# Performance work log

Hardware: AMD Instinct MI355X
Metric: run time of the kernel (lower is better)

The kernel has to match this reference:

```python
import jax, jax.numpy as jnp
import numpy as np

N, E = 50000, 800000
F_IN, C_PRE, C, G_HID = 16, 32, 64, 64
EPS = 1e-5


def graph_norm(x, batch, w, b, ms):
    # PyG GraphNorm over a single graph (batch all zeros)
    cnt = jax.ops.segment_sum(jnp.ones((x.shape[0], 1), x.dtype), batch, num_segments=1)
    mean = jax.ops.segment_sum(x, batch, num_segments=1) / cnt
    out = x - mean[batch] * ms
    var = jax.ops.segment_sum(out * out, batch, num_segments=1) / cnt
    std = jnp.sqrt(var + EPS)
    return w * out / std[batch] + b


def ggnn_conv(h, edge_index, edge_attr,
              gw1, gb1, gw2, gb2, gw3, gb3,
              zw, zb, rw, rb, hw, hb):
    n = h.shape[0]
    loops = jnp.arange(n)
    row = jnp.concatenate([edge_index[0], loops])  # sources (x_j)
    col = jnp.concatenate([edge_index[1], loops])  # targets (x_i), aggregation index
    ea = jnp.concatenate([edge_attr, jnp.ones((n, 1), h.dtype)], axis=0)
    deg = jax.ops.segment_sum(jnp.ones(col.shape[0], h.dtype), col, num_segments=n)
    dis = jnp.where(deg > 0, deg ** -0.5, 0.0)
    norm = dis[row] * dis[col]
    x_j = h[row]
    x_i = h[col]
    g = jnp.concatenate([x_i, x_j, ea], axis=-1)            # [E+N, 2C+1]
    g = jax.nn.relu(g @ gw1 + gb1)
    g = jax.nn.relu(g @ gw2 + gb2)
    gate = jax.nn.sigmoid(g @ gw3 + gb3)                     # [E+N, 1]
    msg = gate * (norm[:, None] * x_j)
    aggr = jax.ops.segment_sum(msg, col, num_segments=n)     # scatter-add
    zi = jnp.concatenate([h, aggr], axis=-1)
    z = jax.nn.sigmoid(zi @ zw + zb)
    r = jax.nn.sigmoid(zi @ rw + rb)
    hc = jax.nn.relu(jnp.concatenate([r * h, aggr], axis=-1) @ hw + hb)
    return (1.0 - z) * h + z * hc


def setup_inputs() -> dict:
    key = jax.random.key(0)
    ks = iter(jax.random.split(key, 40))

    def lin(k, fi, fo):
        return jax.random.normal(k, (fi, fo), jnp.float32) / np.sqrt(fi)

    inp = {
        'x': jax.random.normal(next(ks), (N, F_IN), jnp.float32),
        'edge_index': jax.random.randint(next(ks), (2, E), 0, N),
        'edge_attr': jax.random.uniform(next(ks), (E, 1), jnp.float32),
        'batch': jnp.zeros((N,), jnp.int32),
        'preproc_w': lin(next(ks), F_IN, C_PRE), 'preproc_b': jnp.zeros((C_PRE,), jnp.float32),
        'gn_pre_w': jnp.ones((C_PRE,), jnp.float32), 'gn_pre_b': jnp.zeros((C_PRE,), jnp.float32), 'gn_pre_ms': jnp.ones((C_PRE,), jnp.float32),
        'init_w': lin(next(ks), C_PRE, C), 'init_b': jnp.zeros((C,), jnp.float32),
        'gn_init_w': jnp.ones((C,), jnp.float32), 'gn_init_b': jnp.zeros((C,), jnp.float32), 'gn_init_ms': jnp.ones((C,), jnp.float32),
        'gate_w1': lin(next(ks), 2 * C + 1, G_HID), 'gate_b1': jnp.zeros((G_HID,), jnp.float32),
        'gate_w2': lin(next(ks), G_HID, G_HID), 'gate_b2': jnp.zeros((G_HID,), jnp.float32),
        'gate_w3': lin(next(ks), G_HID, 1), 'gate_b3': jnp.zeros((1,), jnp.float32),
        'lin_z_w': lin(next(ks), 2 * C, C), 'lin_z_b': jnp.zeros((C,), jnp.float32),
        'lin_r_w': lin(next(ks), 2 * C, C), 'lin_r_b': jnp.zeros((C,), jnp.float32),
        'lin_h_w': lin(next(ks), 2 * C, C), 'lin_h_b': jnp.zeros((C,), jnp.float32),
        'gn_ggnn_w': jnp.ones((C,), jnp.float32), 'gn_ggnn_b': jnp.zeros((C,), jnp.float32), 'gn_ggnn_ms': jnp.ones((C,), jnp.float32),
        'fc1_w': lin(next(ks), 2 * C, C), 'fc1_b': jnp.zeros((C,), jnp.float32),
        'gn_fc1_w': jnp.ones((C,), jnp.float32), 'gn_fc1_b': jnp.zeros((C,), jnp.float32), 'gn_fc1_ms': jnp.ones((C,), jnp.float32),
        'fc2_w': lin(next(ks), C, 2), 'fc2_b': jnp.zeros((2,), jnp.float32),
    }
    return inp


def reference(x, edge_index, edge_attr, batch,
              preproc_w, preproc_b, gn_pre_w, gn_pre_b, gn_pre_ms,
              init_w, init_b, gn_init_w, gn_init_b, gn_init_ms,
              gate_w1, gate_b1, gate_w2, gate_b2, gate_w3, gate_b3,
              lin_z_w, lin_z_b, lin_r_w, lin_r_b, lin_h_w, lin_h_b,
              gn_ggnn_w, gn_ggnn_b, gn_ggnn_ms,
              fc1_w, fc1_b, gn_fc1_w, gn_fc1_b, gn_fc1_ms,
              fc2_w, fc2_b):
    n_layers = 4
    h = x @ preproc_w + preproc_b
    h = graph_norm(h, batch, gn_pre_w, gn_pre_b, gn_pre_ms)
    h = jax.nn.relu(h)
    h0 = h @ init_w + init_b
    h0 = graph_norm(h0, batch, gn_init_w, gn_init_b, gn_init_ms)
    h0 = jax.nn.relu(h0)
    h = h0
    for _ in range(n_layers):  # tied GGNN layer
        h = ggnn_conv(h, edge_index, edge_attr,
                      gate_w1, gate_b1, gate_w2, gate_b2, gate_w3, gate_b3,
                      lin_z_w, lin_z_b, lin_r_w, lin_r_b, lin_h_w, lin_h_b)
        h = graph_norm(h, batch, gn_ggnn_w, gn_ggnn_b, gn_ggnn_ms)
    out = jnp.concatenate([h0, h], axis=1)
    out = out @ fc1_w + fc1_b
    out = graph_norm(out, batch, gn_fc1_w, gn_fc1_b, gn_fc1_ms)
    out = jax.nn.relu(out)
    out = out @ fc2_w + fc2_b  # [N, 2] logits
    return out
```

## Files before the change

kernel.cpp:

```cpp
#include <hip/hip_runtime.h>

#define GN_EPS 1e-5f

typedef _Float16 half8 __attribute__((ext_vector_type(8)));
typedef float floatx4 __attribute__((ext_vector_type(4)));

__device__ __forceinline__ float sigmoidf_(float x){ return 1.0f/(1.0f+__expf(-x)); }
__device__ __forceinline__ float bcast_(float v, int k){
  return __int_as_float(__builtin_amdgcn_readlane(__float_as_int(v), k));
}

__global__ void cnt_all_kernel(const int* __restrict__ ei, int* cnt, int E, int n){
  int i = blockIdx.x*blockDim.x+threadIdx.x;
  if (i < n) atomicAdd(&cnt[i], 1);
  if (i < E) atomicAdd(&cnt[ei[E+i]], 1);
}
__global__ __launch_bounds__(256) void scan1_kernel(const int* __restrict__ cnt,
                                                    int* loc, int* bsum,
                                                    float* __restrict__ dis, int n){
  __shared__ int s[256];
  int t = threadIdx.x, i = blockIdx.x*256 + t;
  int v = (i < n) ? cnt[i] : 0;
  if (i < n) dis[i] = rsqrtf((float)v);
  s[t] = v; __syncthreads();
  #pragma unroll
  for (int d = 1; d < 256; d <<= 1){
    int u = (t >= d) ? s[t-d] : 0; __syncthreads();
    s[t] += u; __syncthreads();
  }
  if (i < n) loc[i] = s[t] - v;
  if (t == 255) bsum[blockIdx.x] = s[255];
}
__global__ __launch_bounds__(256) void scan2_kernel(int* bsum, int nb){
  __shared__ int s[256];
  int t = threadIdx.x;
  int v = (t < nb) ? bsum[t] : 0;
  s[t] = v; __syncthreads();
  #pragma unroll
  for (int d = 1; d < 256; d <<= 1){
    int u = (t >= d) ? s[t-d] : 0; __syncthreads();
    s[t] += u; __syncthreads();
  }
  if (t < nb) bsum[t] = s[t] - v;
}
__global__ void scan3_kernel(const int* __restrict__ loc, const int* __restrict__ bsum,
                             int* rowptr, int* fill, int n, int total){
  int i = blockIdx.x*blockDim.x+threadIdx.x;
  if (i < n){ rowptr[i] = loc[i] + bsum[i >> 8]; fill[i] = 0; }
  if (i == 0) rowptr[n] = total;
}
__global__ void scatter_kernel(const int* __restrict__ ei, const float* __restrict__ ea,
                               const int* __restrict__ rowptr, int* fill,
                               unsigned* sd, _Float16* ea2, int E, int n){
  int idx = blockIdx.x*blockDim.x+threadIdx.x;
  int tot = E + n;
  if (idx >= tot) return;
  int r, c; float v;
  if (idx < E){ r = ei[idx]; c = ei[E+idx]; v = ea[idx]; }
  else        { r = c = idx - E; v = 1.0f; }
  int j = rowptr[c] + atomicAdd(&fill[c], 1);
  sd[j] = (unsigned)r | ((unsigned)c << 16);
  ea2[j] = (_Float16)v;
}

__global__ __launch_bounds__(256) void wprep_kernel(
    const float* __restrict__ w1, const float* __restrict__ zw,
    const float* __restrict__ rw, const float* __restrict__ hw,
    const float* __restrict__ fw, const float* __restrict__ w2,
    _Float16* __restrict__ wp){
  int idx = blockIdx.x*256 + threadIdx.x;
  if (idx < 8192){
    int t=idx>>10, kh=(idx>>9)&1, g=(idx>>7)&3, l=(idx>>3)&15, j=idx&7;
    int kg=(t>=4?64:0)+kh*32+g*8+j;
    wp[idx] = (_Float16)w1[kg*64 + (t&3)*16 + l];
  } else if (idx < 40960){
    int m=(idx-8192)>>13, k=(idx-8192)&8191;
    int t=(k>>11)&3, kh=(k>>9)&3, g=(k>>7)&3, l=(k>>3)&15, j=k&7;
    const float* W = (m==0)?zw:((m==1)?rw:((m==2)?hw:fw));
    wp[idx] = (_Float16)W[(kh*32+g*8+j)*64 + t*16 + l];
  } else if (idx < 45056){
    int k = idx-40960;
    int t=(k>>10)&3, kh=(k>>9)&1, g=(k>>7)&3, l=(k>>3)&15, j=k&7;
    wp[idx] = (_Float16)w2[(kh*32+g*8+j)*64 + t*16 + l];
  }
}

template<int K_IN, int C_OUT, int STATS>
__global__ __launch_bounds__(256) void mm1_kernel(
    const float* __restrict__ x, const float* __restrict__ W,
    const float* __restrict__ b, float* __restrict__ y,
    float* __restrict__ stats, int n){
  __shared__ float sW[K_IN*C_OUT];
  __shared__ float sSt[2*C_OUT];
  if (STATS && threadIdx.x < 2*C_OUT) sSt[threadIdx.x] = 0.f;
  for (int i = threadIdx.x; i < K_IN*C_OUT; i += 256) sW[i] = W[i];
  __syncthreads();
  const int lane = threadIdx.x & 63;
  const int col  = (lane < C_OUT) ? lane : 0;
  const float bias = b[col];
  int wid = (blockIdx.x*256 + threadIdx.x) >> 6;
  int nw  = (gridDim.x*256) >> 6;
  float qs = 0.f, qq = 0.f;
  for (int i = wid; i < n; i += nw){
    float xv = (lane < K_IN) ? x[(size_t)i*K_IN + lane] : 0.0f;
    float a0 = bias, a1 = 0.0f;
    #pragma unroll
    for (int k = 0; k < K_IN; k += 2){
      a0 += bcast_(xv, k  ) * sW[(k  )*C_OUT + col];
      a1 += bcast_(xv, k+1) * sW[(k+1)*C_OUT + col];
    }
    if (lane < C_OUT){
      float v = a0 + a1;
      y[(size_t)i*C_OUT + lane] = v;
      if (STATS){ qs += v; qq += v*v; }
    }
  }
  if (STATS){
    if (lane < C_OUT){
      atomicAdd(&sSt[lane], qs);
      atomicAdd(&sSt[C_OUT+lane], qq);
    }
    __syncthreads();
    if (threadIdx.x < 2*C_OUT) atomicAdd(&stats[threadIdx.x], sSt[threadIdx.x]);
  }
}

template<int RELU, int WRITE_H0>
__global__ __launch_bounds__(256) void normpq_kernel(
    const float* __restrict__ hin, float* __restrict__ hout,
    float* __restrict__ h0out,
    const float* __restrict__ stats,
    const float* __restrict__ gw, const float* __restrict__ gb,
    const float* __restrict__ gms,
    const _Float16* __restrict__ w1p, const float* __restrict__ b1,
    _Float16* __restrict__ Ph, _Float16* __restrict__ QH, int n)
{
  __shared__ _Float16 sB[8192];
  __shared__ float sSO[128];
  for (int i = threadIdx.x; i < 1024; i += 256)
    ((half8*)sB)[i] = ((const half8*)w1p)[i];
  if (threadIdx.x < 64){
    int ch = threadIdx.x;
    float invN = 1.0f/(float)n;
    float mean = stats[ch]*invN;
    float mm = mean*gms[ch];
    float var = stats[64+ch]*invN - mm*(2.0f*mean - mm);
    float inv = rsqrtf(fmaxf(var,0.f)+GN_EPS);
    float sc = inv*gw[ch];
    sSO[ch] = sc;
    sSO[64+ch] = gb[ch] - mm*sc;
  }
  __syncthreads();
  const int lane = threadIdx.x & 63;
  const int g16 = lane>>4, l16 = lane&15;
  float scA[8], ofA[8], scB[8], ofB[8];
  #pragma unroll
  for (int j = 0; j < 8; ++j){
    scA[j]=sSO[g16*8+j];    ofA[j]=sSO[64+g16*8+j];
    scB[j]=sSO[32+g16*8+j]; ofB[j]=sSO[96+g16*8+j];
  }
  float b1f[4];
  #pragma unroll
  for (int t = 0; t < 4; ++t) b1f[t] = b1[t*16 + l16];

  int wid = (blockIdx.x*blockDim.x + threadIdx.x) >> 6;
  int nw  = (gridDim.x*blockDim.x) >> 6;
  int tiles = (n + 15) >> 4;
  for (int tile = wid; tile < tiles; tile += nw){
    int base = tile*16;
    int na = min(base + l16, n-1);
    const float* hp = hin + (size_t)na*64;
    float4 a0 = *(const float4*)(hp + g16*8);
    float4 a1 = *(const float4*)(hp + g16*8 + 4);
    float4 c0 = *(const float4*)(hp + 32 + g16*8);
    float4 c1 = *(const float4*)(hp + 32 + g16*8 + 4);
    float va[8] = {a0.x,a0.y,a0.z,a0.w,a1.x,a1.y,a1.z,a1.w};
    float vb[8] = {c0.x,c0.y,c0.z,c0.w,c1.x,c1.y,c1.z,c1.w};
    half8 af0, af1;
    #pragma unroll
    for (int j = 0; j < 8; ++j){
      float v = va[j]*scA[j] + ofA[j];
      if (RELU) v = fmaxf(v, 0.f);
      va[j] = v; af0[j] = (_Float16)v;
      float u = vb[j]*scB[j] + ofB[j];
      if (RELU) u = fmaxf(u, 0.f);
      vb[j] = u; af1[j] = (_Float16)u;
    }
    float* op = hout + (size_t)na*64;
    *(float4*)(op + g16*8)       = (float4){va[0],va[1],va[2],va[3]};
    *(float4*)(op + g16*8 + 4)   = (float4){va[4],va[5],va[6],va[7]};
    *(float4*)(op + 32 + g16*8)  = (float4){vb[0],vb[1],vb[2],vb[3]};
    *(float4*)(op + 32 + g16*8+4)= (float4){vb[4],vb[5],vb[6],vb[7]};
    if (WRITE_H0){
      float* o2 = h0out + (size_t)na*64;
      *(float4*)(o2 + g16*8)       = (float4){va[0],va[1],va[2],va[3]};
      *(float4*)(o2 + g16*8 + 4)   = (float4){va[4],va[5],va[6],va[7]};
      *(float4*)(o2 + 32 + g16*8)  = (float4){vb[0],vb[1],vb[2],vb[3]};
      *(float4*)(o2 + 32 + g16*8+4)= (float4){vb[4],vb[5],vb[6],vb[7]};
    }
    *(half8*)(QH + (size_t)na*128 + 64 + g16*8) = af0;
    *(half8*)(QH + (size_t)na*128 + 96 + g16*8) = af1;

    floatx4 acc[8];
    #pragma unroll
    for (int t = 0; t < 8; ++t){
      float bv = (t < 4) ? b1f[t] : 0.0f;
      acc[t] = (floatx4){bv, bv, bv, bv};
    }
    #pragma unroll
    for (int t = 0; t < 8; ++t){
      half8 bf0 = *(const half8*)&sB[((t*2+0)*4+g16)*128 + l16*8];
      half8 bf1 = *(const half8*)&sB[((t*2+1)*4+g16)*128 + l16*8];
      acc[t] = __builtin_amdgcn_mfma_f32_16x16x32_f16(af0, bf0, acc[t], 0, 0, 0);
      acc[t] = __builtin_amdgcn_mfma_f32_16x16x32_f16(af1, bf1, acc[t], 0, 0, 0);
    }
    #pragma unroll
    for (int t = 0; t < 8; ++t)
      #pragma unroll
      for (int rg = 0; rg < 4; ++rg){
        int nd = base + g16*4 + rg;
        if (nd < n){
          if (t < 4) Ph[(size_t)nd*64  + t*16 + l16]      = (_Float16)acc[t][rg];
          else       QH[(size_t)nd*128 + (t-4)*16 + l16]  = (_Float16)acc[t][rg];
        }
      }
  }
}

__global__ __launch_bounds__(256) void gru_mfma_kernel(
    float* __restrict__ h, float* __restrict__ aggr,
    const float* __restrict__ dis, const _Float16* __restrict__ QH,
    const _Float16* __restrict__ gwp,
    const float* __restrict__ zb, const float* __restrict__ rb,
    const float* __restrict__ hb,
    float* __restrict__ stats, int n)
{
  __shared__ _Float16 sW[3*8192];
  __shared__ _Float16 sRH[4][16][72];
  __shared__ float sSt[128];
  if (threadIdx.x < 128) sSt[threadIdx.x] = 0.f;
  for (int i = threadIdx.x; i < 3072; i += 256)
    ((half8*)sW)[i] = ((const half8*)gwp)[i];
  __syncthreads();
  const int lane = threadIdx.x & 63;
  const int g16 = lane>>4, l16 = lane&15;
  const int w = threadIdx.x >> 6;
  float zbf[4], rbf[4], hbf[4];
  #pragma unroll
  for (int t = 0; t < 4; ++t){
    zbf[t] = zb[t*16+l16]; rbf[t] = rb[t*16+l16]; hbf[t] = hb[t*16+l16];
  }
  float ssum[4] = {0,0,0,0}, ssq[4] = {0,0,0,0};
#define GW(m,t,kh) (*(const half8*)&sW[(m)*8192 + (((t)*4+(kh))*4+g16)*128 + l16*8])

  int wid = (blockIdx.x*blockDim.x + threadIdx.x) >> 6;
  int nw  = (gridDim.x*blockDim.x) >> 6;
  int tiles = (n + 15) >> 4;
  for (int tile = wid; tile < tiles; tile += nw){
    int base = tile*16;
    int na = min(base + l16, n-1);
    float dv = dis[na];
    half8 af[4];
    af[0] = *(const half8*)(QH + (size_t)na*128 + 64 + g16*8);
    af[1] = *(const half8*)(QH + (size_t)na*128 + 96 + g16*8);
    #pragma unroll
    for (int kh = 0; kh < 2; ++kh){
      float* ar = aggr + (size_t)na*64 + kh*32 + g16*8;
      float4 a0 = *(const float4*)ar;
      float4 a1 = *(const float4*)(ar+4);
      *(float4*)(ar)   = (float4){0,0,0,0};
      *(float4*)(ar+4) = (float4){0,0,0,0};
      half8 t8;
      t8[0]=(_Float16)(a0.x*dv); t8[1]=(_Float16)(a0.y*dv);
      t8[2]=(_Float16)(a0.z*dv); t8[3]=(_Float16)(a0.w*dv);
      t8[4]=(_Float16)(a1.x*dv); t8[5]=(_Float16)(a1.y*dv);
      t8[6]=(_Float16)(a1.z*dv); t8[7]=(_Float16)(a1.w*dv);
      af[2+kh] = t8;
    }
    floatx4 az[4], ar4[4];
    #pragma unroll
    for (int t = 0; t < 4; ++t){
      az[t]  = (floatx4){zbf[t], zbf[t], zbf[t], zbf[t]};
      ar4[t] = (floatx4){rbf[t], rbf[t], rbf[t], rbf[t]};
      #pragma unroll
      for (int kh = 0; kh < 4; ++kh){
        az[t]  = __builtin_amdgcn_mfma_f32_16x16x32_f16(af[kh], GW(0,t,kh), az[t],  0, 0, 0);
        ar4[t] = __builtin_amdgcn_mfma_f32_16x16x32_f16(af[kh], GW(1,t,kh), ar4[t], 0, 0, 0);
      }
    }
    float zr[16], hv[16];
    #pragma unroll
    for (int t = 0; t < 4; ++t)
      #pragma unroll
      for (int rg = 0; rg < 4; ++rg){
        int ndc = min(base + g16*4 + rg, n-1);
        float hval = h[(size_t)ndc*64 + t*16 + l16];
        float zv = sigmoidf_(az[t][rg]);
        float rv = sigmoidf_(ar4[t][rg]);
        zr[t*4+rg] = zv; hv[t*4+rg] = hval;
        sRH[w][g16*4+rg][t*16+l16] = (_Float16)(rv*hval);
      }
    asm volatile("s_waitcnt lgkmcnt(0)" ::: "memory");
    __builtin_amdgcn_sched_barrier(0);
    half8 af2_0 = *(const half8*)&sRH[w][l16][g16*8];
    half8 af2_1 = *(const half8*)&sRH[w][l16][32 + g16*8];
    floatx4 ah[4];
    #pragma unroll
    for (int t = 0; t < 4; ++t){
      ah[t] = (floatx4){hbf[t], hbf[t], hbf[t], hbf[t]};
      ah[t] = __builtin_amdgcn_mfma_f32_16x16x32_f16(af2_0, GW(2,t,0), ah[t], 0, 0, 0);
      ah[t] = __builtin_amdgcn_mfma_f32_16x16x32_f16(af2_1, GW(2,t,1), ah[t], 0, 0, 0);
      ah[t] = __builtin_amdgcn_mfma_f32_16x16x32_f16(af[2],  GW(2,t,2), ah[t], 0, 0, 0);
      ah[t] = __builtin_amdgcn_mfma_f32_16x16x32_f16(af[3],  GW(2,t,3), ah[t], 0, 0, 0);
    }
    #pragma unroll
    for (int t = 0; t < 4; ++t)
      #pragma unroll
      for (int rg = 0; rg < 4; ++rg){
        int nd = base + g16*4 + rg;
        if (nd < n){
          float hc = fmaxf(ah[t][rg], 0.f);
          float zv = zr[t*4+rg];
          float hn = (1.f - zv)*hv[t*4+rg] + zv*hc;
          h[(size_t)nd*64 + t*16 + l16] = hn;
          ssum[t] += hn; ssq[t] += hn*hn;
        }
      }
  }
#undef GW
  #pragma unroll
  for (int t = 0; t < 4; ++t){
    atomicAdd(&sSt[t*16+l16], ssum[t]);
    atomicAdd(&sSt[64+t*16+l16], ssq[t]);
  }
  __syncthreads();
  if (threadIdx.x < 128) atomicAdd(&stats[threadIdx.x], sSt[threadIdx.x]);
}

__global__ __launch_bounds__(256) void fc1_mfma_kernel(
    const float* __restrict__ h0, const float* __restrict__ h,
    const _Float16* __restrict__ fp, const float* __restrict__ b,
    float* __restrict__ out, float* __restrict__ stats, int n)
{
  __shared__ _Float16 sB[8192];
  __shared__ float sSt[128];
  if (threadIdx.x < 128) sSt[threadIdx.x] = 0.f;
  for (int i = threadIdx.x; i < 1024; i += 256)
    ((half8*)sB)[i] = ((const half8*)fp)[i];
  __syncthreads();
  const int lane = threadIdx.x & 63;
  const int g16 = lane>>4, l16 = lane&15;
  float bf[4];
  #pragma unroll
  for (int t = 0; t < 4; ++t) bf[t] = b[t*16+l16];
  float ssum[4] = {0,0,0,0}, ssq[4] = {0,0,0,0};

  int wid = (blockIdx.x*blockDim.x + threadIdx.x) >> 6;
  int nw  = (gridDim.x*blockDim.x) >> 6;
  int tiles = (n + 15) >> 4;
  for (int tile = wid; tile < tiles; tile += nw){
    int base = tile*16;
    int na = min(base + l16, n-1);
    half8 af[4];
    #pragma unroll
    for (int kh = 0; kh < 4; ++kh){
      const float* sp = (kh < 2 ? h0 : h) + (size_t)na*64 + (kh&1)*32 + g16*8;
      float4 a0 = *(const float4*)sp;
      float4 a1 = *(const float4*)(sp+4);
      half8 t8;
      t8[0]=(_Float16)a0.x; t8[1]=(_Float16)a0.y; t8[2]=(_Float16)a0.z; t8[3]=(_Float16)a0.w;
      t8[4]=(_Float16)a1.x; t8[5]=(_Float16)a1.y; t8[6]=(_Float16)a1.z; t8[7]=(_Float16)a1.w;
      af[kh] = t8;
    }
    #pragma unroll
    for (int t = 0; t < 4; ++t){
      floatx4 acc = (floatx4){bf[t], bf[t], bf[t], bf[t]};
      #pragma unroll
      for (int kh = 0; kh < 4; ++kh)
        acc = __builtin_amdgcn_mfma_f32_16x16x32_f16(af[kh],
                *(const half8*)&sB[((t*4+kh)*4+g16)*128 + l16*8], acc, 0, 0, 0);
      #pragma unroll
      for (int rg = 0; rg < 4; ++rg){
        int nd = base + g16*4 + rg;
        if (nd < n){
          float v = acc[rg];
          out[(size_t)nd*64 + t*16 + l16] = v;
          ssum[t] += v; ssq[t] += v*v;
        }
      }
    }
  }
  #pragma unroll
  for (int t = 0; t < 4; ++t){
    atomicAdd(&sSt[t*16+l16], ssum[t]);
    atomicAdd(&sSt[64+t*16+l16], ssq[t]);
  }
  __syncthreads();
  if (threadIdx.x < 128) atomicAdd(&stats[threadIdx.x], sSt[threadIdx.x]);
}

__global__ __launch_bounds__(256) void edge_tile_kernel(
    const unsigned* __restrict__ sd, const _Float16* __restrict__ ea2,
    const _Float16* __restrict__ Ph, const _Float16* __restrict__ QH,
    const float* __restrict__ dis,
    const _Float16* __restrict__ w2p, const float* __restrict__ b2,
    const float* __restrict__ w1e, const float* __restrict__ w3,
    const float* __restrict__ b3,
    float* __restrict__ aggr, float* __restrict__ stats, int EN)
{
  __shared__ _Float16 sB[4096];
  if (blockIdx.x == 0 && threadIdx.x < 128) stats[threadIdx.x] = 0.f;
  for (int i = threadIdx.x; i < 512; i += 256)
    ((half8*)sB)[i] = ((const half8*)w2p)[i];
  __syncthreads();

  const int lane = threadIdx.x & 63;
  const int g16  = lane >> 4;
  const int l16  = lane & 15;

  half8 w1h[2];
  #pragma unroll
  for (int kh = 0; kh < 2; ++kh)
    #pragma unroll
    for (int j = 0; j < 8; ++j)
      w1h[kh][j] = (_Float16)w1e[kh*32 + g16*8 + j];

  float w3f[4], b2f[4];
  #pragma unroll
  for (int t = 0; t < 4; ++t){ w3f[t] = w3[t*16 + l16]; b2f[t] = b2[t*16 + l16]; }
  const float b3v = b3[0];
  const _Float16* QHh = QH + 64;

  int wid = (blockIdx.x*blockDim.x + threadIdx.x) >> 6;
  int nw  = (gridDim.x*blockDim.x) >> 6;
  int tiles = (EN + 15) >> 4;

  for (int tile = wid; tile < tiles; tile += nw){
    int e0 = tile << 4;
    int m = EN - e0; if (m > 16) m = 16;
    int el = e0 + ((l16 < m) ? l16 : (m-1));
    unsigned sdv = sd[el];
    int r = (int)(sdv & 0xffffu);
    int c = (int)(sdv >> 16);
    float dv = (l16 < m) ? dis[r] : 0.0f;
    _Float16 eavh = ea2[el];

    half8 hq0 = *(const half8*)(QH + (size_t)r*128 + g16*8);
    half8 hq1 = *(const half8*)(QH + (size_t)r*128 + 32 + g16*8);
    half8 p0  = *(const half8*)(Ph + (size_t)c*64 + g16*8);
    half8 p1  = *(const half8*)(Ph + (size_t)c*64 + 32 + g16*8);

    _Float16 hv16[16];
    #pragma unroll
    for (int i = 0; i < 16; ++i){
      int ri = __builtin_amdgcn_readlane(r, i);
      hv16[i] = QHh[(size_t)ri*128 + lane];
    }

    half8 e8;
    #pragma unroll
    for (int j = 0; j < 8; ++j) e8[j] = eavh;
    half8 a0h = p0 + hq0 + w1h[0]*e8;
    half8 a1h = p1 + hq1 + w1h[1]*e8;
    #pragma unroll
    for (int j = 0; j < 8; ++j){
      a0h[j] = a0h[j] > (_Float16)0.f ? a0h[j] : (_Float16)0.f;
      a1h[j] = a1h[j] > (_Float16)0.f ? a1h[j] : (_Float16)0.f;
    }

    floatx4 acc[4];
    #pragma unroll
    for (int t4 = 0; t4 < 4; ++t4)
      acc[t4] = (floatx4){b2f[t4], b2f[t4], b2f[t4], b2f[t4]};
    __builtin_amdgcn_s_setprio(1);
    #pragma unroll
    for (int t4 = 0; t4 < 4; ++t4){
      half8 bf0 = *(const half8*)&sB[t4*1024 + g16*128 + l16*8];
      half8 bf1 = *(const half8*)&sB[t4*1024 + 512 + g16*128 + l16*8];
      acc[t4] = __builtin_amdgcn_mfma_f32_16x16x32_f16(a0h, bf0, acc[t4], 0, 0, 0);
      acc[t4] = __builtin_amdgcn_mfma_f32_16x16x32_f16(a1h, bf1, acc[t4], 0, 0, 0);
    }
    __builtin_amdgcn_s_setprio(0);

    float s[4] = {0.f,0.f,0.f,0.f};
    #pragma unroll
    for (int t4 = 0; t4 < 4; ++t4)
      #pragma unroll
      for (int rg = 0; rg < 4; ++rg)
        s[rg] += fmaxf(acc[t4][rg], 0.0f) * w3f[t4];
    #pragma unroll
    for (int rg = 0; rg < 4; ++rg){
      #pragma unroll
      for (int off = 1; off < 16; off <<= 1)
        s[rg] += __shfl_xor(s[rg], off);
      s[rg] = sigmoidf_(s[rg] + b3v);
    }

    float fs[4];
    #pragma unroll
    for (int rg = 0; rg < 4; ++rg){
      float dvp = __shfl(dv, (g16 << 4) | (g16*4 + rg));
      fs[rg] = s[rg] * dvp;
    }

    int cnext = __shfl(c, (lane & 48) | ((l16 + 1) & 15));
    unsigned long long bm = __ballot(c != cnext);
    unsigned bmask = ((unsigned)bm | 0x8000u) & 0xffffu;

    float accv = 0.f;
    #pragma unroll
    for (int i = 0; i < 16; ++i){
      float gi = bcast_(fs[i & 3], (i >> 2) << 4);
      accv = fmaf(gi, (float)hv16[i], accv);
      if ((bmask >> i) & 1){
        int ci = __builtin_amdgcn_readlane(c, i);
        atomicAdd(&aggr[(size_t)ci*64 + lane], accv);
        accv = 0.f;
      }
    }
  }
}

template<int C, int RELU>
__global__ __launch_bounds__(256) void norm_apply_kernel(
    const float* __restrict__ x, const float* __restrict__ stats,
    const float* __restrict__ w, const float* __restrict__ b,
    const float* __restrict__ ms, float* __restrict__ y, int n){
  const float invN = 1.0f / (float)n;
  size_t idx = blockIdx.x*256 + threadIdx.x;
  size_t step = (size_t)gridDim.x*256;
  size_t tot = (size_t)n*C;
  for (; idx < tot; idx += step){
    int c = idx % C;
    float mean = stats[c] * invN;
    float mm = mean * ms[c];
    float var = stats[C + c]*invN - mm*(2.0f*mean - mm);
    float inv = rsqrtf(fmaxf(var, 0.0f) + GN_EPS);
    float v = (x[idx] - mm)*inv*w[c] + b[c];
    if (RELU) v = fmaxf(v, 0.0f);
    y[idx] = v;
  }
}

__global__ void fc2_kernel(
    const float* __restrict__ x, const float* __restrict__ w,
    const float* __restrict__ b, float* __restrict__ out, int n){
  int i = blockIdx.x*blockDim.x + threadIdx.x;
  if (i >= n) return;
  float a0 = b[0], a1 = b[1];
  const float4* xr = (const float4*)(x + (size_t)i*64);
  #pragma unroll
  for (int k4 = 0; k4 < 16; ++k4){
    float4 v = xr[k4];
    int k = k4*4;
    a0 += v.x*w[(k+0)*2+0] + v.y*w[(k+1)*2+0] + v.z*w[(k+2)*2+0] + v.w*w[(k+3)*2+0];
    a1 += v.x*w[(k+0)*2+1] + v.y*w[(k+1)*2+1] + v.z*w[(k+2)*2+1] + v.w*w[(k+3)*2+1];
  }
  out[i*2+0] = a0;
  out[i*2+1] = a1;
}

extern "C" void kernel_launch(void* const* d_in, const int* in_sizes, int n_in,
                              void* d_out, int out_size, void* d_ws, size_t ws_size,
                              hipStream_t stream){
  const float* x          = (const float*)d_in[0];
  const int*   ei         = (const int*)  d_in[1];
  const float* ea         = (const float*)d_in[2];
  const float* preproc_w  = (const float*)d_in[4];
  const float* preproc_b  = (const float*)d_in[5];
  const float* gn_pre_w   = (const float*)d_in[6];
  const float* gn_pre_b   = (const float*)d_in[7];
  const float* gn_pre_ms  = (const float*)d_in[8];
  const float* init_w     = (const float*)d_in[9];
  const float* init_b     = (const float*)d_in[10];
  const float* gn_init_w  = (const float*)d_in[11];
  const float* gn_init_b  = (const float*)d_in[12];
  const float* gn_init_ms = (const float*)d_in[13];
  const float* gate_w1    = (const float*)d_in[14];
  const float* gate_b1    = (const float*)d_in[15];
  const float* gate_w2    = (const float*)d_in[16];
  const float* gate_b2    = (const float*)d_in[17];
  const float* gate_w3    = (const float*)d_in[18];
  const float* gate_b3    = (const float*)d_in[19];
  const float* lin_z_w    = (const float*)d_in[20];
  const float* lin_z_b    = (const float*)d_in[21];
  const float* lin_r_w    = (const float*)d_in[22];
  const float* lin_r_b    = (const float*)d_in[23];
  const float* lin_h_w    = (const float*)d_in[24];
  const float* lin_h_b    = (const float*)d_in[25];
  const float* gn_ggnn_w  = (const float*)d_in[26];
  const float* gn_ggnn_b  = (const float*)d_in[27];
  const float* gn_ggnn_ms = (const float*)d_in[28];
  const float* fc1_w      = (const float*)d_in[29];
  const float* fc1_b      = (const float*)d_in[30];
  const float* gn_fc1_w   = (const float*)d_in[31];
  const float* gn_fc1_b   = (const float*)d_in[32];
  const float* gn_fc1_ms  = (const float*)d_in[33];
  const float* fc2_w      = (const float*)d_in[34];
  const float* fc2_b      = (const float*)d_in[35];

  const int N = in_sizes[3];
  const int E = in_sizes[1] / 2;
  const int EN = E + N;

  float* base = (float*)d_ws;
  const size_t R = (size_t)64*N;
  float* h     = base;
  float* h0    = h    + R;
  float* Preg  = h0   + R;
  float* aggr  = Preg + R;
  float* QHreg = aggr + R;
  float* dis   = QHreg + R;
  float* stats = dis + N;
  size_t need = (5*R + N + 128) * sizeof(float);
  if (ws_size < need || N > 65535) return;

  _Float16* Ph  = (_Float16*)Preg;
  _Float16* QH  = (_Float16*)QHreg;
  unsigned* sd  = (unsigned*)(Preg + 32*(size_t)N);
  _Float16* ea2 = (_Float16*)(sd + EN);
  _Float16* wp  = (_Float16*)(((uintptr_t)(ea2 + EN) + 15) & ~(uintptr_t)15);
  _Float16* w1p = wp;
  _Float16* gwp = wp + 8192;
  _Float16* fc1p= wp + 32768;
  _Float16* w2p = wp + 40960;

  int* cnt    = (int*)aggr;
  int* loc    = cnt + N;
  int* fill   = loc + N;
  int* bsum   = fill + N;
  int* rowptr = bsum + 256;

  const int GB = 1024;
  const int RB = 784;
  const int EB = 3072;
  const int nb = (N + 255) / 256;
  const int mNE = (E > N ? E : N);

  hipMemsetAsync(cnt, 0, (size_t)N*sizeof(int), stream);
  cnt_all_kernel<<<(mNE+255)/256, 256, 0, stream>>>(ei, cnt, E, N);
  scan1_kernel<<<nb, 256, 0, stream>>>(cnt, loc, bsum, dis, N);
  scan2_kernel<<<1, 256, 0, stream>>>(bsum, nb);
  scan3_kernel<<<nb, 256, 0, stream>>>(loc, bsum, rowptr, fill, N, EN);
  scatter_kernel<<<(EN+255)/256, 256, 0, stream>>>(ei, ea, rowptr, fill, sd, ea2, E, N);
  wprep_kernel<<<176, 256, 0, stream>>>(gate_w1, lin_z_w, lin_r_w, lin_h_w, fc1_w, gate_w2, wp);
  hipMemsetAsync(aggr, 0, R*sizeof(float), stream);

  hipMemsetAsync(stats, 0, 2*64*sizeof(float), stream);
  mm1_kernel<16,32,1><<<GB, 256, 0, stream>>>(x, preproc_w, preproc_b, h0, stats, N);
  norm_apply_kernel<32,1><<<2048, 256, 0, stream>>>(h0, stats, gn_pre_w, gn_pre_b, gn_pre_ms, h, N);

  hipMemsetAsync(stats, 0, 2*64*sizeof(float), stream);
  mm1_kernel<32,64,1><<<GB, 256, 0, stream>>>(h, init_w, init_b, h0, stats, N);
  normpq_kernel<1,1><<<RB, 256, 0, stream>>>(h0, h, h0, stats,
                                             gn_init_w, gn_init_b, gn_init_ms,
                                             w1p, gate_b1, Ph, QH, N);

  for (int layer = 0; layer < 4; ++layer){
    edge_tile_kernel<<<EB, 256, 0, stream>>>(sd, ea2, Ph, QH, dis,
                                             w2p, gate_b2, gate_w1 + 128*64,
                                             gate_w3, gate_b3, aggr, stats, EN);
    gru_mfma_kernel<<<RB, 256, 0, stream>>>(h, aggr, dis, QH, gwp,
                                            lin_z_b, lin_r_b, lin_h_b, stats, N);
    if (layer < 3)
      normpq_kernel<0,0><<<RB, 256, 0, stream>>>(h, h, nullptr, stats,
                                                 gn_ggnn_w, gn_ggnn_b, gn_ggnn_ms,
                                                 w1p, gate_b1, Ph, QH, N);
    else
      norm_apply_kernel<64,0><<<2048, 256, 0, stream>>>(h, stats, gn_ggnn_w, gn_ggnn_b, gn_ggnn_ms, h, N);
  }

  hipMemsetAsync(stats, 0, 2*64*sizeof(float), stream);
  fc1_mfma_kernel<<<RB, 256, 0, stream>>>(h0, h, fc1p, fc1_b, aggr, stats, N);
  norm_apply_kernel<64,1><<<2048, 256, 0, stream>>>(aggr, stats, gn_fc1_w, gn_fc1_b, gn_fc1_ms, h, N);

  fc2_kernel<<<(N+255)/256, 256, 0, stream>>>(h, fc2_w, fc2_b, (float*)d_out, N);
}
```

Baseline: 645.8 us.

## Fold GraphNorm apply passes into consumer kernels and pack edge records

Eliminates the three standalone norm_apply kernels by computing per-channel scale/offset from stats inside the consuming kernels (mm1, fc1, fc2), applying norm and ReLU on load. Separately packs the edge source, target and fp16 attribute into a 3x16-bit record, replacing a 32-bit sd array plus a separate ea2 array, to cut index bytes in the per-layer edge kernel. This removes several full-tensor read/write passes and launches. The trade-off is a few extra FMAs per element and unaligned 6-byte record loads.

```diff
diff --git a/kernel.cpp b/kernel.cpp
--- a/kernel.cpp
+++ b/kernel.cpp
@@ -9,6 +9,7 @@
 __device__ __forceinline__ float bcast_(float v, int k){
   return __int_as_float(__builtin_amdgcn_readlane(__float_as_int(v), k));
 }
+union hu16 { unsigned short u; _Float16 f; };
 
 __global__ void cnt_all_kernel(const int* __restrict__ ei, int* cnt, int E, int n){
   int i = blockIdx.x*blockDim.x+threadIdx.x;
@@ -51,7 +52,7 @@
 }
 __global__ void scatter_kernel(const int* __restrict__ ei, const float* __restrict__ ea,
                                const int* __restrict__ rowptr, int* fill,
-                               unsigned* sd, _Float16* ea2, int E, int n){
+                               unsigned short* rec, int E, int n){
   int idx = blockIdx.x*blockDim.x+threadIdx.x;
   int tot = E + n;
   if (idx >= tot) return;
@@ -59,8 +60,11 @@
   if (idx < E){ r = ei[idx]; c = ei[E+idx]; v = ea[idx]; }
   else        { r = c = idx - E; v = 1.0f; }
   int j = rowptr[c] + atomicAdd(&fill[c], 1);
-  sd[j] = (unsigned)r | ((unsigned)c << 16);
-  ea2[j] = (_Float16)v;
+  hu16 cv; cv.f = (_Float16)v;
+  size_t b3 = (size_t)j*3;
+  rec[b3]   = (unsigned short)r;
+  rec[b3+1] = (unsigned short)c;
+  rec[b3+2] = cv.u;
 }
 
 __global__ __launch_bounds__(256) void wprep_kernel(
@@ -85,24 +89,41 @@
   }
 }
 
-template<int K_IN, int C_OUT, int STATS>
+template<int K_IN, int C_OUT, int NORMIN, int STATS>
 __global__ __launch_bounds__(256) void mm1_kernel(
     const float* __restrict__ x, const float* __restrict__ W,
-    const float* __restrict__ b, float* __restrict__ y,
-    float* __restrict__ stats, int n){
+    const float* __restrict__ b,
+    const float* __restrict__ nstats, const float* __restrict__ nw,
+    const float* __restrict__ nb, const float* __restrict__ nms,
+    float* __restrict__ y, float* __restrict__ stats, int n){
   __shared__ float sW[K_IN*C_OUT];
   __shared__ float sSt[2*C_OUT];
+  __shared__ float sIN[2*K_IN];
   if (STATS && threadIdx.x < 2*C_OUT) sSt[threadIdx.x] = 0.f;
+  if (NORMIN && threadIdx.x < K_IN){
+    int ch = threadIdx.x;
+    float invN = 1.0f/(float)n;
+    float mean = nstats[ch]*invN;
+    float mm = mean*nms[ch];
+    float var = nstats[K_IN+ch]*invN - mm*(2.0f*mean - mm);
+    float inv = rsqrtf(fmaxf(var,0.f)+GN_EPS);
+    float sc = inv*nw[ch];
+    sIN[ch] = sc;
+    sIN[K_IN+ch] = nb[ch] - mm*sc;
+  }
   for (int i = threadIdx.x; i < K_IN*C_OUT; i += 256) sW[i] = W[i];
   __syncthreads();
   const int lane = threadIdx.x & 63;
   const int col  = (lane < C_OUT) ? lane : 0;
   const float bias = b[col];
+  float isc = 1.f, iof = 0.f;
+  if (NORMIN && lane < K_IN){ isc = sIN[lane]; iof = sIN[K_IN+lane]; }
   int wid = (blockIdx.x*256 + threadIdx.x) >> 6;
-  int nw  = (gridDim.x*256) >> 6;
+  int nw_ = (gridDim.x*256) >> 6;
   float qs = 0.f, qq = 0.f;
-  for (int i = wid; i < n; i += nw){
+  for (int i = wid; i < n; i += nw_){
     float xv = (lane < K_IN) ? x[(size_t)i*K_IN + lane] : 0.0f;
+    if (NORMIN) xv = fmaxf(xv*isc + iof, 0.f);
     float a0 = bias, a1 = 0.0f;
     #pragma unroll
     for (int k = 0; k < K_IN; k += 2){
@@ -339,12 +360,27 @@
 
 __global__ __launch_bounds__(256) void fc1_mfma_kernel(
     const float* __restrict__ h0, const float* __restrict__ h,
+    const float* __restrict__ hstats,
+    const float* __restrict__ gw, const float* __restrict__ gb,
+    const float* __restrict__ gms,
     const _Float16* __restrict__ fp, const float* __restrict__ b,
     float* __restrict__ out, float* __restrict__ stats, int n)
 {
   __shared__ _Float16 sB[8192];
   __shared__ float sSt[128];
+  __shared__ float sSO[128];
   if (threadIdx.x < 128) sSt[threadIdx.x] = 0.f;
+  if (threadIdx.x < 64){
+    int ch = threadIdx.x;
+    float invN = 1.0f/(float)n;
+    float mean = hstats[ch]*invN;
+    float mm = mean*gms[ch];
+    float var = hstats[64+ch]*invN - mm*(2.0f*mean - mm);
+    float inv = rsqrtf(fmaxf(var,0.f)+GN_EPS);
+    float sc = inv*gw[ch];
+    sSO[ch] = sc;
+    sSO[64+ch] = gb[ch] - mm*sc;
+  }
   for (int i = threadIdx.x; i < 1024; i += 256)
     ((half8*)sB)[i] = ((const half8*)fp)[i];
   __syncthreads();
@@ -353,6 +389,12 @@
   float bf[4];
   #pragma unroll
   for (int t = 0; t < 4; ++t) bf[t] = b[t*16+l16];
+  float scH[16], ofH[16];
+  #pragma unroll
+  for (int j = 0; j < 8; ++j){
+    scH[j]   = sSO[g16*8+j];    ofH[j]   = sSO[64+g16*8+j];
+    scH[8+j] = sSO[32+g16*8+j]; ofH[8+j] = sSO[96+g16*8+j];
+  }
   float ssum[4] = {0,0,0,0}, ssq[4] = {0,0,0,0};
 
   int wid = (blockIdx.x*blockDim.x + threadIdx.x) >> 6;
@@ -367,9 +409,16 @@
       const float* sp = (kh < 2 ? h0 : h) + (size_t)na*64 + (kh&1)*32 + g16*8;
       float4 a0 = *(const float4*)sp;
       float4 a1 = *(const float4*)(sp+4);
+      float v[8] = {a0.x,a0.y,a0.z,a0.w,a1.x,a1.y,a1.z,a1.w};
       half8 t8;
-      t8[0]=(_Float16)a0.x; t8[1]=(_Float16)a0.y; t8[2]=(_Float16)a0.z; t8[3]=(_Float16)a0.w;
-      t8[4]=(_Float16)a1.x; t8[5]=(_Float16)a1.y; t8[6]=(_Float16)a1.z; t8[7]=(_Float16)a1.w;
+      if (kh < 2){
+        #pragma unroll
+        for (int j = 0; j < 8; ++j) t8[j] = (_Float16)v[j];
+      } else {
+        #pragma unroll
+        for (int j = 0; j < 8; ++j)
+          t8[j] = (_Float16)(v[j]*scH[(kh&1)*8+j] + ofH[(kh&1)*8+j]);
+      }
       af[kh] = t8;
     }
     #pragma unroll
@@ -400,7 +449,7 @@
 }
 
 __global__ __launch_bounds__(256) void edge_tile_kernel(
-    const unsigned* __restrict__ sd, const _Float16* __restrict__ ea2,
+    const unsigned short* __restrict__ rec,
     const _Float16* __restrict__ Ph, const _Float16* __restrict__ QH,
     const float* __restrict__ dis,
     const _Float16* __restrict__ w2p, const float* __restrict__ b2,
@@ -439,11 +488,12 @@
     int e0 = tile << 4;
     int m = EN - e0; if (m > 16) m = 16;
     int el = e0 + ((l16 < m) ? l16 : (m-1));
-    unsigned sdv = sd[el];
-    int r = (int)(sdv & 0xffffu);
-    int c = (int)(sdv >> 16);
+    size_t b3i = (size_t)el*3;
+    int r = rec[b3i];
+    int c = rec[b3i+1];
+    hu16 cv; cv.u = rec[b3i+2];
+    _Float16 eavh = cv.f;
     float dv = (l16 < m) ? dis[r] : 0.0f;
-    _Float16 eavh = ea2[el];
 
     half8 hq0 = *(const half8*)(QH + (size_t)r*128 + g16*8);
     half8 hq1 = *(const half8*)(QH + (size_t)r*128 + 32 + g16*8);
@@ -521,30 +571,27 @@
   }
 }
 
-template<int C, int RELU>
-__global__ __launch_bounds__(256) void norm_apply_kernel(
+__global__ __launch_bounds__(256) void fc2_kernel(
     const float* __restrict__ x, const float* __restrict__ stats,
+    const float* __restrict__ gw, const float* __restrict__ gb,
+    const float* __restrict__ gms,
     const float* __restrict__ w, const float* __restrict__ b,
-    const float* __restrict__ ms, float* __restrict__ y, int n){
-  const float invN = 1.0f / (float)n;
-  size_t idx = blockIdx.x*256 + threadIdx.x;
-  size_t step = (size_t)gridDim.x*256;
-  size_t tot = (size_t)n*C;
-  for (; idx < tot; idx += step){
-    int c = idx % C;
-    float mean = stats[c] * invN;
-    float mm = mean * ms[c];
-    float var = stats[C + c]*invN - mm*(2.0f*mean - mm);
-    float inv = rsqrtf(fmaxf(var, 0.0f) + GN_EPS);
-    float v = (x[idx] - mm)*inv*w[c] + b[c];
-    if (RELU) v = fmaxf(v, 0.0f);
-    y[idx] = v;
-  }
-}
-
-__global__ void fc2_kernel(
-    const float* __restrict__ x, const float* __restrict__ w,
-    const float* __restrict__ b, float* __restrict__ out, int n){
+    float* __restrict__ out, int n){
+  __shared__ float sSO[128];
+  __shared__ float sW[128];
+  if (threadIdx.x < 64){
+    int ch = threadIdx.x;
+    float invN = 1.0f/(float)n;
+    float mean = stats[ch]*invN;
+    float mm = mean*gms[ch];
+    float var = stats[64+ch]*invN - mm*(2.0f*mean - mm);
+    float inv = rsqrtf(fmaxf(var,0.f)+GN_EPS);
+    float sc = inv*gw[ch];
+    sSO[ch] = sc;
+    sSO[64+ch] = gb[ch] - mm*sc;
+  }
+  for (int k = threadIdx.x; k < 128; k += 256) sW[k] = w[k];
+  __syncthreads();
   int i = blockIdx.x*blockDim.x + threadIdx.x;
   if (i >= n) return;
   float a0 = b[0], a1 = b[1];
@@ -552,9 +599,14 @@
   #pragma unroll
   for (int k4 = 0; k4 < 16; ++k4){
     float4 v = xr[k4];
-    int k = k4*4;
-    a0 += v.x*w[(k+0)*2+0] + v.y*w[(k+1)*2+0] + v.z*w[(k+2)*2+0] + v.w*w[(k+3)*2+0];
-    a1 += v.x*w[(k+0)*2+1] + v.y*w[(k+1)*2+1] + v.z*w[(k+2)*2+1] + v.w*w[(k+3)*2+1];
+    float vv[4] = {v.x, v.y, v.z, v.w};
+    #pragma unroll
+    for (int j = 0; j < 4; ++j){
+      int k = k4*4 + j;
+      float u = fmaxf(vv[j]*sSO[k] + sSO[64+k], 0.f);
+      a0 += u*sW[k*2+0];
+      a1 += u*sW[k*2+1];
+    }
   }
   out[i*2+0] = a0;
   out[i*2+1] = a1;
@@ -612,14 +664,13 @@
   float* QHreg = aggr + R;
   float* dis   = QHreg + R;
   float* stats = dis + N;
-  size_t need = (5*R + N + 128) * sizeof(float);
+  size_t need = (5*R + N + 256) * sizeof(float);
   if (ws_size < need || N > 65535) return;
 
   _Float16* Ph  = (_Float16*)Preg;
   _Float16* QH  = (_Float16*)QHreg;
-  unsigned* sd  = (unsigned*)(Preg + 32*(size_t)N);
-  _Float16* ea2 = (_Float16*)(sd + EN);
-  _Float16* wp  = (_Float16*)(((uintptr_t)(ea2 + EN) + 15) & ~(uintptr_t)15);
+  unsigned short* rec = (unsigned short*)(Preg + 32*(size_t)N);
+  _Float16* wp  = (_Float16*)(((uintptr_t)(rec + (size_t)EN*3) + 15) & ~(uintptr_t)15);
   _Float16* w1p = wp;
   _Float16* gwp = wp + 8192;
   _Float16* fc1p= wp + 32768;
@@ -642,22 +693,23 @@
   scan1_kernel<<<nb, 256, 0, stream>>>(cnt, loc, bsum, dis, N);
   scan2_kernel<<<1, 256, 0, stream>>>(bsum, nb);
   scan3_kernel<<<nb, 256, 0, stream>>>(loc, bsum, rowptr, fill, N, EN);
-  scatter_kernel<<<(EN+255)/256, 256, 0, stream>>>(ei, ea, rowptr, fill, sd, ea2, E, N);
+  scatter_kernel<<<(EN+255)/256, 256, 0, stream>>>(ei, ea, rowptr, fill, rec, E, N);
   wprep_kernel<<<176, 256, 0, stream>>>(gate_w1, lin_z_w, lin_r_w, lin_h_w, fc1_w, gate_w2, wp);
   hipMemsetAsync(aggr, 0, R*sizeof(float), stream);
 
-  hipMemsetAsync(stats, 0, 2*64*sizeof(float), stream);
-  mm1_kernel<16,32,1><<<GB, 256, 0, stream>>>(x, preproc_w, preproc_b, h0, stats, N);
-  norm_apply_kernel<32,1><<<2048, 256, 0, stream>>>(h0, stats, gn_pre_w, gn_pre_b, gn_pre_ms, h, N);
-
-  hipMemsetAsync(stats, 0, 2*64*sizeof(float), stream);
-  mm1_kernel<32,64,1><<<GB, 256, 0, stream>>>(h, init_w, init_b, h0, stats, N);
-  normpq_kernel<1,1><<<RB, 256, 0, stream>>>(h0, h, h0, stats,
+  hipMemsetAsync(stats, 0, 2*128*sizeof(float), stream);
+  mm1_kernel<16,32,0,1><<<GB, 256, 0, stream>>>(x, preproc_w, preproc_b,
+                                                nullptr, nullptr, nullptr, nullptr,
+                                                h, stats, N);
+  mm1_kernel<32,64,1,1><<<GB, 256, 0, stream>>>(h, init_w, init_b,
+                                                stats, gn_pre_w, gn_pre_b, gn_pre_ms,
+                                                h0, stats + 128, N);
+  normpq_kernel<1,1><<<RB, 256, 0, stream>>>(h0, h, h0, stats + 128,
                                              gn_init_w, gn_init_b, gn_init_ms,
                                              w1p, gate_b1, Ph, QH, N);
 
   for (int layer = 0; layer < 4; ++layer){
-    edge_tile_kernel<<<EB, 256, 0, stream>>>(sd, ea2, Ph, QH, dis,
+    edge_tile_kernel<<<EB, 256, 0, stream>>>(rec, Ph, QH, dis,
                                              w2p, gate_b2, gate_w1 + 128*64,
                                              gate_w3, gate_b3, aggr, stats, EN);
     gru_mfma_kernel<<<RB, 256, 0, stream>>>(h, aggr, dis, QH, gwp,
@@ -666,13 +718,14 @@
       normpq_kernel<0,0><<<RB, 256, 0, stream>>>(h, h, nullptr, stats,
                                                  gn_ggnn_w, gn_ggnn_b, gn_ggnn_ms,
                                                  w1p, gate_b1, Ph, QH, N);
-    else
-      norm_apply_kernel<64,0><<<2048, 256, 0, stream>>>(h, stats, gn_ggnn_w, gn_ggnn_b, gn_ggnn_ms, h, N);
-  }
-
-  hipMemsetAsync(stats, 0, 2*64*sizeof(float), stream);
-  fc1_mfma_kernel<<<RB, 256, 0, stream>>>(h0, h, fc1p, fc1_b, aggr, stats, N);
-  norm_apply_kernel<64,1><<<2048, 256, 0, stream>>>(aggr, stats, gn_fc1_w, gn_fc1_b, gn_fc1_ms, h, N);
-
-  fc2_kernel<<<(N+255)/256, 256, 0, stream>>>(h, fc2_w, fc2_b, (float*)d_out, N);
-}
+  }
+
+  hipMemsetAsync(stats + 128, 0, 128*sizeof(float), stream);
+  fc1_mfma_kernel<<<RB, 256, 0, stream>>>(h0, h, stats,
+                                          gn_ggnn_w, gn_ggnn_b, gn_ggnn_ms,
+                                          fc1p, fc1_b, aggr, stats + 128, N);
+
+  fc2_kernel<<<(N+255)/256, 256, 0, stream>>>(aggr, stats + 128,
+                                              gn_fc1_w, gn_fc1_b, gn_fc1_ms,
+                                              fc2_w, fc2_b, (float*)d_out, N);
+}
```

After: 630.7 us. 2.3% less time.
